# Performance work log

Measured on AMD Instinct MI355X. Metric: run time of the kernel, lower is better.

The kernel has to match this reference:

```python
import jax, jax.numpy as jnp
import numpy as np

L, D, H, DK, S, B = 6, 1024, 16, 64, 512, 8
DFF = 4 * D
NEG = -1.0e9


def layer_norm(x, g, b, eps=1e-5):
    mu = jnp.mean(x, axis=-1, keepdims=True)
    var = jnp.var(x, axis=-1, keepdims=True)
    return (x - mu) * jax.lax.rsqrt(var + eps) * g + b


def setup_inputs() -> dict:
    key = jax.random.key(0)
    ks = jax.random.split(key, 16)
    s = 0.02
    inp = {
        "x": jax.random.normal(ks[0], (B, S, D), jnp.float32),
        "mask": jax.random.bernoulli(ks[1], 0.1, (B, S, S)),
        "relation": jax.random.normal(ks[2], (B, S, S), jnp.float32) * 0.1,
        # per-layer params (stacked over L)
        "Wq": jax.random.normal(ks[3], (L, D, H * DK), jnp.float32) * s,
        "Wk": jax.random.normal(ks[4], (L, D, H * DK), jnp.float32) * s,
        "Wv": jax.random.normal(ks[5], (L, D, H * DK), jnp.float32) * s,
        "Wo": jax.random.normal(ks[6], (L, H * DK, D), jnp.float32) * s,
        "bo": jnp.zeros((L, D), jnp.float32),
        "ln_g": jnp.ones((L, D), jnp.float32),   # EncoderLayer.norm (shared pre-attn / pre-FFN)
        "ln_b": jnp.zeros((L, D), jnp.float32),
        "ln2_g": jnp.ones((L, D), jnp.float32),  # AttSubLayerv2.norm
        "ln2_b": jnp.zeros((L, D), jnp.float32),
        "W1": jax.random.normal(ks[7], (L, D, DFF), jnp.float32) * s,
        "b1": jnp.zeros((L, DFF), jnp.float32),
        "W2": jax.random.normal(ks[8], (L, DFF, D), jnp.float32) * s,
        "b2": jnp.zeros((L, D), jnp.float32),
        "lnf_g": jnp.ones((D,), jnp.float32),    # Encoder.norm
        "lnf_b": jnp.zeros((D,), jnp.float32),
    }
    return inp


def reference(x, mask, relation, Wq, Wk, Wv, Wo, bo, ln_g, ln_b, ln2_g, ln2_b,
              W1, b1, W2, b2, lnf_g, lnf_b):
    # dropout layers run in eval mode (identity)
    scale = 1.0 / jnp.sqrt(jnp.asarray(DK, x.dtype))
    h = x
    attns = []
    for l in range(L):
        q_in = layer_norm(h, ln_g[l], ln_b[l])
        # AttSubLayerv2
        def proj(W):
            return jnp.einsum('bsd,de->bse', q_in, W).reshape(h.shape[0], -1, H, DK).transpose(0, 2, 1, 3)
        Q, K, V = proj(Wq[l]), proj(Wk[l]), proj(Wv[l])  # [B,H,S,DK]
        qk = jnp.einsum('bhqd,bhkd->bhqk', Q, K)
        scores = jnp.einsum('bhqk,bkn->bhqn', qk, relation) * scale
        scores = jnp.where(mask[:, None], NEG, scores)
        p = jax.nn.softmax(scores, axis=-1)  # [B,H,S,S]
        att = jnp.einsum('bhqk,bhkd->bhqd', p, V).transpose(0, 2, 1, 3).reshape(h.shape[0], -1, H * DK)
        att = att @ Wo[l] + bo[l]
        att_out = layer_norm(att + q_in, ln2_g[l], ln2_b[l])
        h = h + att_out
        # FFN (pre-norm with shared EncoderLayer norm)
        f = layer_norm(h, ln_g[l], ln_b[l])
        h = h + (jax.nn.relu(f @ W1[l] + b1[l]) @ W2[l] + b2[l])
        attns.append(p)
    out = layer_norm(h, lnf_g, lnf_b)
    return out, jnp.stack(attns)
```

## Files before the change

### kernel.cpp

```cpp
#include <hip/hip_runtime.h>
#include <hip/hip_bf16.h>
#include <stdint.h>

#define LL 6
#define DD 1024
#define HH 16
#define DKK 64
#define SS 512
#define BB 8
#define DFF_ 4096
#define BS (BB*SS)
#define NEGV -1.0e9f

typedef __attribute__((ext_vector_type(8))) short short8;
typedef __attribute__((ext_vector_type(4))) float f32x4;
typedef __attribute__((ext_vector_type(4))) unsigned short ushort4v;

static __device__ __forceinline__ float bf2f(unsigned short u){
  union { unsigned int i; float f; } v; v.i = ((unsigned int)u)<<16; return v.f;
}
static __device__ __forceinline__ unsigned short f2bf(float f){
  union { float f; unsigned int i; } v; v.f=f;
  unsigned int r = v.i + 0x7fff + ((v.i>>16)&1);
  return (unsigned short)(r>>16);
}

static __device__ __forceinline__ void gload16(const void* g, void* l){
  __builtin_amdgcn_global_load_lds((const __attribute__((address_space(1))) unsigned int*)g,
                                   (__attribute__((address_space(3))) unsigned int*)l, 16, 0, 0);
}

struct TrDesc { const float* in; unsigned short* out; long is1,is2,os1,os2; int ldin,ldout,zd,gx,gy; };
struct TrPack { TrDesc d[7]; int cum[8]; };

__global__ void __launch_bounds__(256) tr_multi_k(TrPack P)
{
  __shared__ float t[32][33];
  int bid=blockIdx.x, di=0;
  #pragma unroll
  for(int k=1;k<7;k++) if(bid>=P.cum[k]) di=k;
  TrDesc dd=P.d[di];
  int local=bid-P.cum[di];
  int bx=local%dd.gx; int rest=local/dd.gx;
  int by=rest%dd.gy; int z=rest/dd.gy;
  int z1=z/dd.zd, z2=z%dd.zd;
  const float* ip=dd.in+z1*dd.is1+z2*dd.is2;
  unsigned short* op=dd.out+z1*dd.os1+z2*dd.os2;
  int r0=by*32, c0=bx*32;
  int tx=threadIdx.x, ty=threadIdx.y;
  #pragma unroll
  for(int i=0;i<4;i++)
    t[ty+i*8][tx] = ip[(long)(r0+ty+i*8)*dd.ldin + c0+tx];
  __syncthreads();
  #pragma unroll
  for(int i=0;i<4;i++)
    op[(long)(c0+ty+i*8)*dd.ldout + r0+tx] = f2bf(t[tx][ty+i*8]);
}

__global__ void __launch_bounds__(256) maskpack_k(const int* __restrict__ mask, unsigned* __restrict__ mb)
{
  int idx = blockIdx.x*256 + threadIdx.x;
  int row = idx>>4, w = idx&15;
  const int* mp = mask + (long)row*SS + w*32;
  unsigned v=0;
  #pragma unroll
  for(int i=0;i<32;i++) v |= (mp[i]!=0) ? (1u<<i) : 0u;
  mb[idx]=v;
}

__global__ void __launch_bounds__(256) ln_k(const float* __restrict__ src,
    const float* __restrict__ gw, const float* __restrict__ bw,
    float* __restrict__ outf, unsigned short* __restrict__ outb,
    const float* __restrict__ resid)
{
  long row=blockIdx.x;
  float4 v=((const float4*)(src+row*DD))[threadIdx.x];
  float s=v.x+v.y+v.z+v.w;
  float s2=v.x*v.x+v.y*v.y+v.z*v.z+v.w*v.w;
  #pragma unroll
  for(int o=32;o;o>>=1){ s+=__shfl_xor(s,o); s2+=__shfl_xor(s2,o); }
  __shared__ float red[8];
  int wid=threadIdx.x>>6, lane=threadIdx.x&63;
  if(lane==0){ red[wid]=s; red[4+wid]=s2; }
  __syncthreads();
  s=red[0]+red[1]+red[2]+red[3];
  s2=red[4]+red[5]+red[6]+red[7];
  float mu=s*(1.f/DD);
  float rstd=rsqrtf(s2*(1.f/DD)-mu*mu+1e-5f);
  int c=threadIdx.x*4;
  float4 g4=*(const float4*)(gw+c), b4=*(const float4*)(bw+c);
  float4 o;
  o.x=(v.x-mu)*rstd*g4.x+b4.x;
  o.y=(v.y-mu)*rstd*g4.y+b4.y;
  o.z=(v.z-mu)*rstd*g4.z+b4.z;
  o.w=(v.w-mu)*rstd*g4.w+b4.w;
  if(resid){
    float4 r4=((const float4*)(resid+row*DD))[threadIdx.x];
    o.x+=r4.x; o.y+=r4.y; o.z+=r4.z; o.w+=r4.w;
  }
  if(outf) ((float4*)(outf+row*DD))[threadIdx.x]=o;
  if(outb){
    uint2 pk;
    pk.x=(unsigned)f2bf(o.x)|((unsigned)f2bf(o.y)<<16);
    pk.y=(unsigned)f2bf(o.z)|((unsigned)f2bf(o.w)<<16);
    ((uint2*)(outb+row*DD))[threadIdx.x]=pk;
  }
}

__global__ void __launch_bounds__(256) ln2_k(const float* __restrict__ src,
    const float* __restrict__ resid,
    const float* __restrict__ g2, const float* __restrict__ b2,
    const float* __restrict__ g1, const float* __restrict__ b1,
    float* __restrict__ outf, unsigned short* __restrict__ outb)
{
  long row=blockIdx.x;
  int wid=threadIdx.x>>6, lane=threadIdx.x&63, c=threadIdx.x*4;
  __shared__ float red[8];
  float4 v=((const float4*)(src+row*DD))[threadIdx.x];
  float s=v.x+v.y+v.z+v.w;
  float s2=v.x*v.x+v.y*v.y+v.z*v.z+v.w*v.w;
  #pragma unroll
  for(int o=32;o;o>>=1){ s+=__shfl_xor(s,o); s2+=__shfl_xor(s2,o); }
  if(lane==0){ red[wid]=s; red[4+wid]=s2; }
  __syncthreads();
  s=red[0]+red[1]+red[2]+red[3];
  s2=red[4]+red[5]+red[6]+red[7];
  float mu=s*(1.f/DD);
  float rstd=rsqrtf(s2*(1.f/DD)-mu*mu+1e-5f);
  float4 g4=*(const float4*)(g2+c), b4=*(const float4*)(b2+c);
  float4 r4=((const float4*)(resid+row*DD))[threadIdx.x];
  float4 o;
  o.x=(v.x-mu)*rstd*g4.x+b4.x+r4.x;
  o.y=(v.y-mu)*rstd*g4.y+b4.y+r4.y;
  o.z=(v.z-mu)*rstd*g4.z+b4.z+r4.z;
  o.w=(v.w-mu)*rstd*g4.w+b4.w+r4.w;
  ((float4*)(outf+row*DD))[threadIdx.x]=o;
  s=o.x+o.y+o.z+o.w;
  s2=o.x*o.x+o.y*o.y+o.z*o.z+o.w*o.w;
  #pragma unroll
  for(int of=32;of;of>>=1){ s+=__shfl_xor(s,of); s2+=__shfl_xor(s2,of); }
  __syncthreads();
  if(lane==0){ red[wid]=s; red[4+wid]=s2; }
  __syncthreads();
  s=red[0]+red[1]+red[2]+red[3];
  s2=red[4]+red[5]+red[6]+red[7];
  mu=s*(1.f/DD);
  rstd=rsqrtf(s2*(1.f/DD)-mu*mu+1e-5f);
  g4=*(const float4*)(g1+c); b4=*(const float4*)(b1+c);
  uint2 pk;
  pk.x=(unsigned)f2bf((o.x-mu)*rstd*g4.x+b4.x)|((unsigned)f2bf((o.y-mu)*rstd*g4.y+b4.y)<<16);
  pk.y=(unsigned)f2bf((o.z-mu)*rstd*g4.z+b4.z)|((unsigned)f2bf((o.w-mu)*rstd*g4.w+b4.w)<<16);
  ((uint2*)(outb+row*DD))[threadIdx.x]=pk;
}

struct GemmP {
  const unsigned short* A; long sA1,sA2; int ldA;
  const unsigned short* B; long sB1,sB2; int ldB;
  float* outF; unsigned short* outB; long sO1,sO2; int ldO;
  const float* bias;
  const float* residF; long sR1,sR2; int ldR;
  const unsigned short* residB;
  unsigned short *kt, *vt;
  int K, ZD, relu, qkv;
};

template<int BM,int BN,int WM,int WN>
__global__ void __launch_bounds__(WM*WN*64) gemm_k(GemmP p)
{
  constexpr int BK=32, NT=WM*WN*64;
  constexpr int FM=BM/WM/16, FN=BN/WN/16;
  __shared__ __align__(16) unsigned short As[BM*BK];
  __shared__ __align__(16) unsigned short Bs[BN*BK];
  int z=blockIdx.z, z1=z/p.ZD, z2=z%p.ZD;
  const unsigned short* Ap = p.A + z1*p.sA1 + z2*p.sA2;
  const unsigned short* Bp = p.B + z1*p.sB1 + z2*p.sB2;
  int m0=blockIdx.y*BM, n0=blockIdx.x*BN;
  int tid=threadIdx.x, lane=tid&63, wid=tid>>6;
  int wr=wid/WN, wc=wid%WN;
  f32x4 acc[FM][FN];
  #pragma unroll
  for(int i=0;i<FM;i++)
    #pragma unroll
    for(int j=0;j<FN;j++) acc[i][j]=(f32x4){0.f,0.f,0.f,0.f};
  const int lr=lane&15, lk=(lane>>4)*8;
  for(int k0=0;k0<p.K;k0+=BK){
    #pragma unroll
    for(int r=0;r<(BM*4)/NT;r++){
      int v=r*NT+wid*64+lane;
      gload16(Ap + (long)(m0+(v>>2))*p.ldA + k0 + (v&3)*8, As + (r*NT+wid*64)*8);
    }
    #pragma unroll
    for(int r=0;r<(BN*4)/NT;r++){
      int v=r*NT+wid*64+lane;
      gload16(Bp + (long)(n0+(v>>2))*p.ldB + k0 + (v&3)*8, Bs + (r*NT+wid*64)*8);
    }
    __syncthreads();
    short8 af[FM], bfr[FN];
    #pragma unroll
    for(int i=0;i<FM;i++) af[i]=*(const short8*)(As + (wr*(BM/WM)+i*16+lr)*BK + lk);
    #pragma unroll
    for(int j=0;j<FN;j++) bfr[j]=*(const short8*)(Bs + (wc*(BN/WN)+j*16+lr)*BK + lk);
    #pragma unroll
    for(int i=0;i<FM;i++)
      #pragma unroll
      for(int j=0;j<FN;j++)
        acc[i][j]=__builtin_amdgcn_mfma_f32_16x16x32_bf16(af[i],bfr[j],acc[i][j],0,0,0);
    __syncthreads();
  }
  int rl=(lane>>4)*4;
  if(p.qkv){
    #pragma unroll
    for(int i=0;i<FM;i++){
      int gr0 = m0 + wr*(BM/WM) + i*16 + rl;
      int b = gr0>>9, s0 = gr0&511;
      #pragma unroll
      for(int j=0;j<FN;j++){
        int gcb = n0 + wc*(BN/WN) + j*16;
        int gc = gcb + lr;
        if(gcb < 1024){
          #pragma unroll
          for(int r=0;r<4;r++)
            p.outB[(long)(gr0+r)*1024 + gc] = f2bf(acc[i][j][r]);
        } else {
          unsigned short* dst = gcb<2048 ? p.kt : p.vt;
          int hh=(gc>>6)&15, d=gc&63;
          ushort4v pk;
          pk.x=f2bf(acc[i][j][0]); pk.y=f2bf(acc[i][j][1]);
          pk.z=f2bf(acc[i][j][2]); pk.w=f2bf(acc[i][j][3]);
          *(ushort4v*)(dst + (((long)b*HH+hh)*DKK+d)*SS + s0) = pk;
        }
      }
    }
    return;
  }
  #pragma unroll
  for(int i=0;i<FM;i++){
    int gr0 = m0 + wr*(BM/WM) + i*16 + rl;
    #pragma unroll
    for(int j=0;j<FN;j++){
      int gc = n0 + wc*(BN/WN) + j*16 + lr;
      float bv = p.bias ? p.bias[gc] : 0.f;
      #pragma unroll
      for(int r=0;r<4;r++){
        long ro=(long)(gr0+r);
        float val=acc[i][j][r]+bv;
        if(p.relu) val=fmaxf(val,0.f);
        if(p.residF) val += p.residF[z1*p.sR1+z2*p.sR2+ro*(long)p.ldR+gc];
        if(p.residB) val += bf2f(p.residB[ro*(long)p.ldR+gc]);
        long oo = z1*p.sO1+z2*p.sO2+ro*(long)p.ldO+gc;
        if(p.outF) p.outF[oo]=val;
        if(p.outB) p.outB[oo]=f2bf(val);
      }
    }
  }
}

template<int BM,int BN,int WM,int WN>
static inline void launch_gemm(const GemmP& p,int M,int N,int Z,hipStream_t s){
  gemm_k<BM,BN,WM,WN><<<dim3(N/BN,M/BM,Z),dim3(WM*WN*64),0,s>>>(p);
}

__global__ void __launch_bounds__(512) att_k(const unsigned short* __restrict__ Qb,
    const unsigned short* __restrict__ KRT, float* __restrict__ pout,
    const unsigned* __restrict__ maskb, const unsigned short* __restrict__ Vt,
    unsigned short* __restrict__ attb)
{
  constexpr int BM=128, BK=32, NT=512;
  constexpr int FM=4, FN=8;
  __shared__ __align__(16) char smem[49152];
  unsigned short* As = (unsigned short*)smem;
  unsigned short* Bs = (unsigned short*)(smem+8192);
  unsigned short* Ps = (unsigned short*)smem;
  unsigned short* Vs = (unsigned short*)(smem+32768);
  __shared__ float redmx[BM][4];
  __shared__ float redsm[BM][4];
  int bh = blockIdx.y; int b = bh>>4, h = bh&15;
  const unsigned short* Ap = Qb + (long)b*SS*1024 + h*64;
  const unsigned short* Bp = KRT + (long)bh*SS*DKK;
  int m0 = blockIdx.x*BM;
  int tid=threadIdx.x, lane=tid&63, wid=tid>>6;
  int wr=wid>>2, wc=wid&3;
  f32x4 acc[FM][FN];
  #pragma unroll
  for(int i=0;i<FM;i++)
    #pragma unroll
    for(int j=0;j<FN;j++) acc[i][j]=(f32x4){0.f,0.f,0.f,0.f};
  const int lr=lane&15, lk=(lane>>4)*8;
  for(int k0=0;k0<DKK;k0+=BK){
    { int v=tid;
      gload16(Ap + (long)(m0+(v>>2))*1024 + k0 + (v&3)*8, As + (wid*64)*8); }
    #pragma unroll
    for(int r=0;r<4;r++){
      int v=r*NT+tid;
      gload16(Bp + (long)(v>>2)*DKK + k0 + (v&3)*8, Bs + (r*NT+wid*64)*8);
    }
    __syncthreads();
    short8 af[FM], bfr[FN];
    #pragma unroll
    for(int i=0;i<FM;i++) af[i]=*(const short8*)(As + (wr*64+i*16+lr)*BK + lk);
    #pragma unroll
    for(int j=0;j<FN;j++) bfr[j]=*(const short8*)(Bs + (wc*128+j*16+lr)*BK + lk);
    #pragma unroll
    for(int i=0;i<FM;i++)
      #pragma unroll
      for(int j=0;j<FN;j++)
        acc[i][j]=__builtin_amdgcn_mfma_f32_16x16x32_bf16(af[i],bfr[j],acc[i][j],0,0,0);
    __syncthreads();
  }
  const int rl=(lane>>4)*4;
  #pragma unroll
  for(int i=0;i<FM;i++){
    #pragma unroll
    for(int r=0;r<4;r++){
      int row=wr*64+i*16+rl+r;
      uint4 mw = *((const uint4*)(maskb + ((long)(b*SS+m0+row))*16 + wc*4));
      float m_=-3.4e38f;
      #pragma unroll
      for(int j=0;j<FN;j++){
        unsigned word = (j>>1)==0? mw.x : (j>>1)==1? mw.y : (j>>1)==2? mw.z : mw.w;
        float v = ((word>>(((j&1)<<4)+lr))&1) ? NEGV : acc[i][j][r]*0.125f;
        acc[i][j][r]=v; m_=fmaxf(m_,v);
      }
      #pragma unroll
      for(int o=1;o<16;o<<=1) m_=fmaxf(m_,__shfl_xor(m_,o));
      if(lr==0) redmx[row][wc]=m_;
    }
  }
  __syncthreads();
  #pragma unroll
  for(int i=0;i<FM;i++){
    #pragma unroll
    for(int r=0;r<4;r++){
      int row=wr*64+i*16+rl+r;
      float m_=fmaxf(fmaxf(redmx[row][0],redmx[row][1]),fmaxf(redmx[row][2],redmx[row][3]));
      float s_=0.f;
      #pragma unroll
      for(int j=0;j<FN;j++){
        float e=__expf(acc[i][j][r]-m_);
        acc[i][j][r]=e; s_+=e;
      }
      #pragma unroll
      for(int o=1;o<16;o<<=1) s_+=__shfl_xor(s_,o);
      if(lr==0) redsm[row][wc]=s_;
    }
  }
  __syncthreads();
  #pragma unroll
  for(int i=0;i<FM;i++){
    #pragma unroll
    for(int r=0;r<4;r++){
      int row=wr*64+i*16+rl+r;
      float inv=1.f/(redsm[row][0]+redsm[row][1]+redsm[row][2]+redsm[row][3]);
      long obase=((long)bh*SS + m0+row)*(long)SS;
      #pragma unroll
      for(int j=0;j<FN;j++){
        int col=wc*128+j*16+lr;
        float pv=acc[i][j][r]*inv;
        acc[i][j][r]=pv;
        pout[obase+col]=pv;
      }
    }
  }
  __syncthreads();
  f32x4 attacc[4];
  #pragma unroll
  for(int j=0;j<4;j++) attacc[j]=(f32x4){0.f,0.f,0.f,0.f};
  for(int kc=0;kc<4;kc++){
    #pragma unroll
    for(int r2=0;r2<2;r2++){
      int v=r2*512+tid;
      int d=v>>4, m=v&15;
      int u=m^(d&7);
      gload16(Vt + ((long)bh*64 + d)*512 + kc*128 + u*8, Vs + (r2*512 + wid*64)*8);
    }
    if(wc==kc){
      #pragma unroll
      for(int i=0;i<FM;i++){
        #pragma unroll
        for(int r=0;r<4;r++){
          int row=wr*64+i*16+rl+r;
          #pragma unroll
          for(int j=0;j<FN;j++){
            int col=j*16+lr;
            Ps[row*128 + (col ^ ((row&7)<<3))] = f2bf(acc[i][j][r]);
          }
        }
      }
    }
    __syncthreads();
    #pragma unroll
    for(int kk=0;kk<4;kk++){
      int arow=wid*16+lr;
      short8 paf=*(const short8*)(Ps + arow*128 + ((kk*32+lk) ^ ((arow&7)<<3)));
      #pragma unroll
      for(int j=0;j<4;j++){
        int d=j*16+lr;
        short8 vbf=*(const short8*)(Vs + d*128 + ((kk*32+lk) ^ ((d&7)<<3)));
        attacc[j]=__builtin_amdgcn_mfma_f32_16x16x32_bf16(paf,vbf,attacc[j],0,0,0);
      }
    }
    __syncthreads();
  }
  #pragma unroll
  for(int j=0;j<4;j++){
    #pragma unroll
    for(int r=0;r<4;r++){
      int row = m0 + wid*16 + rl + r;
      attb[((long)b*SS + row)*DD + h*64 + j*16 + lr] = f2bf(attacc[j][r]);
    }
  }
}

extern "C" void kernel_launch(void* const* d_in, const int* in_sizes, int n_in,
                              void* d_out, int out_size, void* d_ws, size_t ws_size,
                              hipStream_t stream)
{
  const float* x    =(const float*)d_in[0];
  const int*   mask =(const int*)d_in[1];
  const float* rel  =(const float*)d_in[2];
  const float* Wq   =(const float*)d_in[3];
  const float* Wk   =(const float*)d_in[4];
  const float* Wv   =(const float*)d_in[5];
  const float* Wo   =(const float*)d_in[6];
  const float* bo   =(const float*)d_in[7];
  const float* ln_g =(const float*)d_in[8];
  const float* ln_b =(const float*)d_in[9];
  const float* ln2_g=(const float*)d_in[10];
  const float* ln2_b=(const float*)d_in[11];
  const float* W1   =(const float*)d_in[12];
  const float* b1   =(const float*)d_in[13];
  const float* W2   =(const float*)d_in[14];
  const float* b2   =(const float*)d_in[15];
  const float* lnf_g=(const float*)d_in[16];
  const float* lnf_b=(const float*)d_in[17];
  float* out=(float*)d_out;

  char* w=(char*)d_ws;
  auto alloc=[&](long bytes)->void*{ void* p=(void*)w; w += (bytes+255)&~255L; return p; };
  unsigned short* WTqkv=(unsigned short*)alloc((long)LL*3072*1024*2);
  unsigned short* WoT  =(unsigned short*)alloc((long)LL*1024*1024*2);
  unsigned short* W1T  =(unsigned short*)alloc((long)LL*DFF_*DD*2);
  unsigned short* W2T  =(unsigned short*)alloc((long)LL*DD*DFF_*2);
  unsigned short* relT =(unsigned short*)alloc((long)BB*SS*SS*2);
  unsigned short* qin_b=(unsigned short*)alloc((long)BS*DD*2);
  unsigned short* Qb   =(unsigned short*)alloc((long)BS*1024*2);
  unsigned short* Vt   =(unsigned short*)alloc((long)BB*HH*DKK*SS*2);
  unsigned short* Kt   =(unsigned short*)alloc((long)BB*HH*DKK*SS*2);
  unsigned short* KRT  =(unsigned short*)alloc((long)BB*HH*SS*DKK*2);
  unsigned short* attb =(unsigned short*)alloc((long)BS*DD*2);
  float*          attres=(float*)alloc((long)BS*DD*4);
  unsigned short* gbuf =(unsigned short*)alloc((long)BS*DFF_*2);
  float*          hbuf =(float*)alloc((long)BS*DD*4);
  unsigned*       maskb=(unsigned*)alloc((long)BS*16*4);
  (void)ws_size; (void)in_sizes; (void)n_in; (void)out_size;

  TrPack tp;
  auto set=[&](int i, const float* in, unsigned short* o, int ldin, int ldout,
               long is1, long os1, int zd, long is2, long os2, int gx, int gy){
    tp.d[i]={in,o,is1,is2,os1,os2,ldin,ldout,zd,gx,gy};
  };
  set(0, Wq, WTqkv,           1024,1024,(long)1024*1024,(long)3072*1024,1,0,0, 32,32);
  set(1, Wk, WTqkv+1024*1024, 1024,1024,(long)1024*1024,(long)3072*1024,1,0,0, 32,32);
  set(2, Wv, WTqkv+2048*1024, 1024,1024,(long)1024*1024,(long)3072*1024,1,0,0, 32,32);
  set(3, Wo, WoT,             1024,1024,(long)1024*1024,(long)1024*1024,1,0,0, 32,32);
  set(4, W1, W1T, 4096,1024,(long)1024*4096,(long)1024*4096,1,0,0, 128,32);
  set(5, W2, W2T, 1024,4096,(long)4096*1024,(long)4096*1024,1,0,0, 32,128);
  set(6, rel, relT, 512,512,(long)512*512,(long)512*512,1,0,0, 16,16);
  int nb[7]={32*32*LL,32*32*LL,32*32*LL,32*32*LL,128*32*LL,32*128*LL,16*16*BB};
  tp.cum[0]=0;
  for(int i=0;i<7;i++) tp.cum[i+1]=tp.cum[i]+nb[i];
  tr_multi_k<<<dim3(tp.cum[7]),dim3(32,8),0,stream>>>(tp);
  maskpack_k<<<dim3(BS*16/256),dim3(256),0,stream>>>(mask, maskb);

  const float* hin = x;
  for(int l=0;l<LL;l++){
    ln_k<<<dim3(BS),dim3(256),0,stream>>>(hin, ln_g+l*DD, ln_b+l*DD, (float*)nullptr, qin_b, (const float*)nullptr);
    { GemmP p{}; p.A=qin_b; p.ldA=DD; p.B=WTqkv+(long)l*3072*1024; p.ldB=DD;
      p.outB=Qb; p.kt=Kt; p.vt=Vt; p.qkv=1; p.K=DD; p.ZD=1;
      launch_gemm<128,128,2,2>(p, BS, 3072, 1, stream); }
    { GemmP p{}; p.A=relT; p.sA1=(long)SS*SS; p.sA2=0; p.ldA=SS;
      p.B=Kt; p.sB1=(long)HH*DKK*SS; p.sB2=(long)DKK*SS; p.ldB=SS;
      p.outB=KRT; p.sO1=(long)HH*SS*DKK; p.sO2=(long)SS*DKK; p.ldO=DKK;
      p.K=SS; p.ZD=HH;
      launch_gemm<128,64,2,2>(p, SS, DKK, BB*HH, stream); }
    float* attn_l = out + (long)BS*DD + (long)l*BB*HH*SS*SS;
    att_k<<<dim3(SS/128, BB*HH),dim3(512),0,stream>>>(Qb, KRT, attn_l, maskb, Vt, attb);
    { GemmP p{}; p.A=attb; p.ldA=DD; p.B=WoT+(long)l*1024*1024; p.ldB=DD;
      p.outF=attres; p.ldO=DD; p.bias=bo+l*DD;
      p.residB=qin_b; p.ldR=DD; p.K=DD; p.ZD=1;
      launch_gemm<64,128,2,2>(p, BS, DD, 1, stream); }
    ln2_k<<<dim3(BS),dim3(256),0,stream>>>(attres, hin, ln2_g+l*DD, ln2_b+l*DD,
        ln_g+l*DD, ln_b+l*DD, hbuf, qin_b);
    { GemmP p{}; p.A=qin_b; p.ldA=DD; p.B=W1T+(long)l*DFF_*DD; p.ldB=DD;
      p.outB=gbuf; p.ldO=DFF_; p.bias=b1+l*DFF_; p.relu=1; p.K=DD; p.ZD=1;
      launch_gemm<128,128,2,2>(p, BS, DFF_, 1, stream); }
    { GemmP p{}; p.A=gbuf; p.ldA=DFF_; p.B=W2T+(long)l*DD*DFF_; p.ldB=DFF_;
      p.outF=hbuf; p.ldO=DD; p.bias=b2+l*DD;
      p.residF=hbuf; p.ldR=DD; p.K=DFF_; p.ZD=1;
      launch_gemm<64,128,2,2>(p, BS, DD, 1, stream); }
    hin=hbuf;
  }
  ln_k<<<dim3(BS),dim3(256),0,stream>>>(hbuf, lnf_g, lnf_b, out, (unsigned short*)nullptr, (const float*)nullptr);
}
```

Measured before the change: 2.390 ms.

## Add triple-buffered 128x256 GEMM with swizzled LDS for dense projections

Adds a new bf16 MFMA GEMM kernel that uses 128x256 tiles with BK=64 and 8 waves. It keeps three LDS stages in flight with manual vmcnt waits and raw barriers, and XOR-swizzles the LDS columns to avoid bank conflicts. The QKV, Wo, W1 and W2 projections are routed to this kernel, and the QKV scatter epilogue moves out of the generic GEMM into it. Deeper prefetch and larger tiles are meant to hide global-load latency and raise MFMA utilisation, at the cost of more LDS per block and fewer blocks for the N=1024 GEMMs (4x32 grid).

```diff
diff --git a/kernel.cpp b/kernel.cpp
--- a/kernel.cpp
+++ b/kernel.cpp
@@ -208,31 +208,6 @@
     __syncthreads();
   }
   int rl=(lane>>4)*4;
-  if(p.qkv){
-    #pragma unroll
-    for(int i=0;i<FM;i++){
-      int gr0 = m0 + wr*(BM/WM) + i*16 + rl;
-      int b = gr0>>9, s0 = gr0&511;
-      #pragma unroll
-      for(int j=0;j<FN;j++){
-        int gcb = n0 + wc*(BN/WN) + j*16;
-        int gc = gcb + lr;
-        if(gcb < 1024){
-          #pragma unroll
-          for(int r=0;r<4;r++)
-            p.outB[(long)(gr0+r)*1024 + gc] = f2bf(acc[i][j][r]);
-        } else {
-          unsigned short* dst = gcb<2048 ? p.kt : p.vt;
-          int hh=(gc>>6)&15, d=gc&63;
-          ushort4v pk;
-          pk.x=f2bf(acc[i][j][0]); pk.y=f2bf(acc[i][j][1]);
-          pk.z=f2bf(acc[i][j][2]); pk.w=f2bf(acc[i][j][3]);
-          *(ushort4v*)(dst + (((long)b*HH+hh)*DKK+d)*SS + s0) = pk;
-        }
-      }
-    }
-    return;
-  }
   #pragma unroll
   for(int i=0;i<FM;i++){
     int gr0 = m0 + wr*(BM/WM) + i*16 + rl;
@@ -258,6 +233,141 @@
 template<int BM,int BN,int WM,int WN>
 static inline void launch_gemm(const GemmP& p,int M,int N,int Z,hipStream_t s){
   gemm_k<BM,BN,WM,WN><<<dim3(N/BN,M/BM,Z),dim3(WM*WN*64),0,s>>>(p);
+}
+
+template<int MODE>
+__global__ void __launch_bounds__(512,2) gemm8_k(GemmP p)
+{
+  constexpr int BM=128, BN=256, BK=64;
+  constexpr int BUFE=(BM+BN)*BK;
+  __shared__ __align__(16) unsigned short smem[3*BUFE];
+  const int tid=threadIdx.x, lane=tid&63, wid=tid>>6;
+  const int wr=wid>>2, wc=wid&3;
+  const int lr=lane&15, lk=(lane>>4)*8;
+  const int m0=blockIdx.y*BM, n0=blockIdx.x*BN;
+  const int NT=p.K/BK;
+  const unsigned short* Ap=p.A;
+  const unsigned short* Bp=p.B;
+
+  const int sr8 = lane>>3;
+  const int scol = ((lane&7)*8) ^ ((sr8&4)?16:0);
+
+  #define STAGE8(T,BI) { \
+    const long kb_=(long)(T)*BK; \
+    unsigned short* As_=smem+(BI)*BUFE; \
+    unsigned short* Bs_=As_+BM*BK; \
+    _Pragma("unroll") \
+    for(int L=0;L<2;L++){ \
+      int r_=L*64+wid*8+sr8; \
+      gload16(Ap+(long)(m0+r_)*p.ldA+kb_+scol, As_+L*4096+wid*512); \
+    } \
+    _Pragma("unroll") \
+    for(int L=0;L<4;L++){ \
+      int r_=L*64+wid*8+sr8; \
+      gload16(Bp+(long)(n0+r_)*p.ldB+kb_+scol, Bs_+L*4096+wid*512); \
+    } }
+
+  f32x4 acc[4][4];
+  #pragma unroll
+  for(int m=0;m<4;m++)
+    #pragma unroll
+    for(int n=0;n<4;n++) acc[m][n]=(f32x4){0.f,0.f,0.f,0.f};
+
+  STAGE8(0,0);
+  STAGE8(1,1);
+  asm volatile("s_waitcnt vmcnt(6)" ::: "memory");
+  __builtin_amdgcn_sched_barrier(0);
+  __builtin_amdgcn_s_barrier();
+  __builtin_amdgcn_sched_barrier(0);
+
+  const int xr = (lr&4)?16:0;
+  for(int t=0;t<NT;t++){
+    if(t+2<NT) STAGE8(t+2,(t+2)%3);
+    const unsigned short* As=smem+(t%3)*BUFE;
+    const unsigned short* Bs=As+BM*BK;
+    short8 a[4][2], b[4][2];
+    #pragma unroll
+    for(int m=0;m<4;m++){
+      int r=wr*64+m*16+lr;
+      #pragma unroll
+      for(int kk=0;kk<2;kk++)
+        a[m][kk]=*(const short8*)(As + r*BK + ((kk*32+lk)^xr));
+    }
+    #pragma unroll
+    for(int n=0;n<4;n++){
+      int c=wc*64+n*16+lr;
+      #pragma unroll
+      for(int kk=0;kk<2;kk++)
+        b[n][kk]=*(const short8*)(Bs + c*BK + ((kk*32+lk)^xr));
+    }
+    __builtin_amdgcn_s_setprio(1);
+    #pragma unroll
+    for(int kk=0;kk<2;kk++)
+      #pragma unroll
+      for(int m=0;m<4;m++)
+        #pragma unroll
+        for(int n=0;n<4;n++)
+          acc[m][n]=__builtin_amdgcn_mfma_f32_16x16x32_bf16(a[m][kk],b[n][kk],acc[m][n],0,0,0);
+    __builtin_amdgcn_s_setprio(0);
+    if(t+2<NT) asm volatile("s_waitcnt vmcnt(6)" ::: "memory");
+    else       asm volatile("s_waitcnt vmcnt(0)" ::: "memory");
+    __builtin_amdgcn_sched_barrier(0);
+    __builtin_amdgcn_s_barrier();
+    __builtin_amdgcn_sched_barrier(0);
+  }
+  #undef STAGE8
+
+  const int rl=(lane>>4)*4;
+  if(MODE==1){
+    int sec = n0>>10;
+    #pragma unroll
+    for(int m=0;m<4;m++){
+      int gr0 = m0 + wr*64 + m*16 + rl;
+      int b = gr0>>9, s0 = gr0&511;
+      #pragma unroll
+      for(int n=0;n<4;n++){
+        int gc = n0 + wc*64 + n*16 + lr;
+        if(sec==0){
+          #pragma unroll
+          for(int r=0;r<4;r++)
+            p.outB[(long)(gr0+r)*1024 + gc] = f2bf(acc[m][n][r]);
+        } else {
+          unsigned short* dst = sec==1 ? p.kt : p.vt;
+          int hh=(gc>>6)&15, d=gc&63;
+          ushort4v pk;
+          pk.x=f2bf(acc[m][n][0]); pk.y=f2bf(acc[m][n][1]);
+          pk.z=f2bf(acc[m][n][2]); pk.w=f2bf(acc[m][n][3]);
+          *(ushort4v*)(dst + (((long)b*HH+hh)*DKK+d)*SS + s0) = pk;
+        }
+      }
+    }
+  } else {
+    #pragma unroll
+    for(int m=0;m<4;m++){
+      int gr0 = m0 + wr*64 + m*16 + rl;
+      #pragma unroll
+      for(int n=0;n<4;n++){
+        int gc = n0 + wc*64 + n*16 + lr;
+        float bv = p.bias ? p.bias[gc] : 0.f;
+        #pragma unroll
+        for(int r=0;r<4;r++){
+          long ro=(long)(gr0+r);
+          float val=acc[m][n][r]+bv;
+          if(p.relu) val=fmaxf(val,0.f);
+          if(p.residF) val += p.residF[ro*(long)p.ldR+gc];
+          if(p.residB) val += bf2f(p.residB[ro*(long)p.ldR+gc]);
+          long oo = ro*(long)p.ldO+gc;
+          if(p.outF) p.outF[oo]=val;
+          if(p.outB) p.outB[oo]=f2bf(val);
+        }
+      }
+    }
+  }
+}
+
+template<int MODE>
+static inline void launch_gemm8(const GemmP& p,int M,int N,hipStream_t s){
+  gemm8_k<MODE><<<dim3(N/256,M/128),dim3(512),0,s>>>(p);
 }
 
 __global__ void __launch_bounds__(512) att_k(const unsigned short* __restrict__ Qb,
@@ -476,8 +586,8 @@
   for(int l=0;l<LL;l++){
     ln_k<<<dim3(BS),dim3(256),0,stream>>>(hin, ln_g+l*DD, ln_b+l*DD, (float*)nullptr, qin_b, (const float*)nullptr);
     { GemmP p{}; p.A=qin_b; p.ldA=DD; p.B=WTqkv+(long)l*3072*1024; p.ldB=DD;
-      p.outB=Qb; p.kt=Kt; p.vt=Vt; p.qkv=1; p.K=DD; p.ZD=1;
-      launch_gemm<128,128,2,2>(p, BS, 3072, 1, stream); }
+      p.outB=Qb; p.kt=Kt; p.vt=Vt; p.K=DD;
+      launch_gemm8<1>(p, BS, 3072, stream); }
     { GemmP p{}; p.A=relT; p.sA1=(long)SS*SS; p.sA2=0; p.ldA=SS;
       p.B=Kt; p.sB1=(long)HH*DKK*SS; p.sB2=(long)DKK*SS; p.ldB=SS;
       p.outB=KRT; p.sO1=(long)HH*SS*DKK; p.sO2=(long)SS*DKK; p.ldO=DKK;
@@ -487,17 +597,17 @@
     att_k<<<dim3(SS/128, BB*HH),dim3(512),0,stream>>>(Qb, KRT, attn_l, maskb, Vt, attb);
     { GemmP p{}; p.A=attb; p.ldA=DD; p.B=WoT+(long)l*1024*1024; p.ldB=DD;
       p.outF=attres; p.ldO=DD; p.bias=bo+l*DD;
-      p.residB=qin_b; p.ldR=DD; p.K=DD; p.ZD=1;
-      launch_gemm<64,128,2,2>(p, BS, DD, 1, stream); }
+      p.residB=qin_b; p.ldR=DD; p.K=DD;
+      launch_gemm8<0>(p, BS, DD, stream); }
     ln2_k<<<dim3(BS),dim3(256),0,stream>>>(attres, hin, ln2_g+l*DD, ln2_b+l*DD,
         ln_g+l*DD, ln_b+l*DD, hbuf, qin_b);
     { GemmP p{}; p.A=qin_b; p.ldA=DD; p.B=W1T+(long)l*DFF_*DD; p.ldB=DD;
-      p.outB=gbuf; p.ldO=DFF_; p.bias=b1+l*DFF_; p.relu=1; p.K=DD; p.ZD=1;
-      launch_gemm<128,128,2,2>(p, BS, DFF_, 1, stream); }
+      p.outB=gbuf; p.ldO=DFF_; p.bias=b1+l*DFF_; p.relu=1; p.K=DD;
+      launch_gemm8<0>(p, BS, DFF_, stream); }
     { GemmP p{}; p.A=gbuf; p.ldA=DFF_; p.B=W2T+(long)l*DD*DFF_; p.ldB=DFF_;
       p.outF=hbuf; p.ldO=DD; p.bias=b2+l*DD;
-      p.residF=hbuf; p.ldR=DD; p.K=DFF_; p.ZD=1;
-      launch_gemm<64,128,2,2>(p, BS, DD, 1, stream); }
+      p.residF=hbuf; p.ldR=DD; p.K=DFF_;
+      launch_gemm8<0>(p, BS, DD, stream); }
     hin=hbuf;
   }
   ln_k<<<dim3(BS),dim3(256),0,stream>>>(hbuf, lnf_g, lnf_b, out, (unsigned short*)nullptr, (const float*)nullptr);
```

Result: faster. 2.236 ms (-6.4%).

## Rewrite GEMM with double-buffered LDS, XOR swizzle, larger tiles, grouped block order

Applied to the files above, without the earlier changes.

Replaces the single-buffered BK=32 GEMM with a double-buffered BK=64 kernel. The next K tile is prefetched while MFMAs run on the current one, LDS is XOR-swizzled to avoid bank conflicts, and a remapped 1D grid groups blocks for better L2 reuse. Larger 256x256 tiles with 8 waves are used for the QKV and FFN1 GEMMs. The relation x K GEMM is batched per batch across all heads, writing KRT in a [B,S,1024] layout that att_k now reads with stride 1024. This adds more LDS per block and more register pressure from the larger tiles, which may limit occupancy.

```diff
diff --git a/kernel.cpp b/kernel.cpp
--- a/kernel.cpp
+++ b/kernel.cpp
@@ -154,110 +154,143 @@
 }
 
 struct GemmP {
-  const unsigned short* A; long sA1,sA2; int ldA;
-  const unsigned short* B; long sB1,sB2; int ldB;
-  float* outF; unsigned short* outB; long sO1,sO2; int ldO;
+  const unsigned short* A; long sA1; int ldA;
+  const unsigned short* B; long sB1; int ldB;
+  float* outF; unsigned short* outB; long sO1; int ldO;
   const float* bias;
-  const float* residF; long sR1,sR2; int ldR;
+  const float* residF; int ldR;
   const unsigned short* residB;
   unsigned short *kt, *vt;
-  int K, ZD, relu, qkv;
+  int K, relu, mb;
 };
 
-template<int BM,int BN,int WM,int WN>
-__global__ void __launch_bounds__(WM*WN*64) gemm_k(GemmP p)
-{
-  constexpr int BK=32, NT=WM*WN*64;
-  constexpr int FM=BM/WM/16, FN=BN/WN/16;
-  __shared__ __align__(16) unsigned short As[BM*BK];
-  __shared__ __align__(16) unsigned short Bs[BN*BK];
-  int z=blockIdx.z, z1=z/p.ZD, z2=z%p.ZD;
-  const unsigned short* Ap = p.A + z1*p.sA1 + z2*p.sA2;
-  const unsigned short* Bp = p.B + z1*p.sB1 + z2*p.sB2;
-  int m0=blockIdx.y*BM, n0=blockIdx.x*BN;
-  int tid=threadIdx.x, lane=tid&63, wid=tid>>6;
-  int wr=wid/WN, wc=wid%WN;
+template<int MODE,int BM,int BN,int WM,int WN>
+__global__ void __launch_bounds__(WM*WN*64,2) gemm2p_k(GemmP p)
+{
+  constexpr int NW=WM*WN, BK=64;
+  constexpr int WRT=BM/WM, WCT=BN/WN;
+  constexpr int FM=WRT/16, FN=WCT/16;
+  constexpr int RG=NW*8;
+  constexpr int BUFE=(BM+BN)*BK;
+  __shared__ __align__(16) unsigned short smem[2*BUFE];
+  const int tid=threadIdx.x, lane=tid&63, wid=tid>>6;
+  const int wr=wid/WN, wc=wid%WN;
+  const int lr=lane&15, lk=(lane>>4)*8;
+  const int nwg=gridDim.x, bid=blockIdx.x;
+  const int nb=(bid&7)*(nwg>>3)+(bid>>3);
+  const int m0=(nb%p.mb)*BM, n0=(nb/p.mb)*BN;
+  const int z=blockIdx.y;
+  const unsigned short* Ap=p.A+(long)z*p.sA1;
+  const unsigned short* Bp=p.B+(long)z*p.sB1;
+  const int NT=p.K/BK;
+
+  const int sr8=lane>>3;
+  const int scol=((lane&7)^sr8)<<3;
+
+  #define STG(T,BI) { \
+    const long kb_=(long)(T)*BK; \
+    unsigned short* As_=smem+(BI)*BUFE; \
+    unsigned short* Bs_=As_+BM*BK; \
+    _Pragma("unroll") \
+    for(int L=0;L<BM/RG;L++){ int r_=L*RG+wid*8+sr8; \
+      gload16(Ap+(long)(m0+r_)*p.ldA+kb_+scol, As_+(L*RG+wid*8)*BK); } \
+    _Pragma("unroll") \
+    for(int L=0;L<BN/RG;L++){ int r_=L*RG+wid*8+sr8; \
+      gload16(Bp+(long)(n0+r_)*p.ldB+kb_+scol, Bs_+(L*RG+wid*8)*BK); } }
+
   f32x4 acc[FM][FN];
   #pragma unroll
-  for(int i=0;i<FM;i++)
-    #pragma unroll
-    for(int j=0;j<FN;j++) acc[i][j]=(f32x4){0.f,0.f,0.f,0.f};
-  const int lr=lane&15, lk=(lane>>4)*8;
-  for(int k0=0;k0<p.K;k0+=BK){
-    #pragma unroll
-    for(int r=0;r<(BM*4)/NT;r++){
-      int v=r*NT+wid*64+lane;
-      gload16(Ap + (long)(m0+(v>>2))*p.ldA + k0 + (v&3)*8, As + (r*NT+wid*64)*8);
-    }
-    #pragma unroll
-    for(int r=0;r<(BN*4)/NT;r++){
-      int v=r*NT+wid*64+lane;
-      gload16(Bp + (long)(n0+(v>>2))*p.ldB + k0 + (v&3)*8, Bs + (r*NT+wid*64)*8);
-    }
-    __syncthreads();
-    short8 af[FM], bfr[FN];
-    #pragma unroll
-    for(int i=0;i<FM;i++) af[i]=*(const short8*)(As + (wr*(BM/WM)+i*16+lr)*BK + lk);
-    #pragma unroll
-    for(int j=0;j<FN;j++) bfr[j]=*(const short8*)(Bs + (wc*(BN/WN)+j*16+lr)*BK + lk);
-    #pragma unroll
-    for(int i=0;i<FM;i++)
-      #pragma unroll
-      for(int j=0;j<FN;j++)
-        acc[i][j]=__builtin_amdgcn_mfma_f32_16x16x32_bf16(af[i],bfr[j],acc[i][j],0,0,0);
-    __syncthreads();
-  }
-  int rl=(lane>>4)*4;
-  if(p.qkv){
-    #pragma unroll
-    for(int i=0;i<FM;i++){
-      int gr0 = m0 + wr*(BM/WM) + i*16 + rl;
+  for(int m=0;m<FM;m++)
+    #pragma unroll
+    for(int n=0;n<FN;n++) acc[m][n]=(f32x4){0.f,0.f,0.f,0.f};
+
+  STG(0,0);
+  asm volatile("s_waitcnt vmcnt(0)" ::: "memory");
+  __builtin_amdgcn_sched_barrier(0);
+  __builtin_amdgcn_s_barrier();
+  __builtin_amdgcn_sched_barrier(0);
+
+  const int xr=(lr&7)<<3;
+  int cur=0;
+  for(int t=0;t<NT;t++){
+    if(t+1<NT) STG(t+1,cur^1);
+    const unsigned short* As=smem+cur*BUFE;
+    const unsigned short* Bs=As+BM*BK;
+    #pragma unroll
+    for(int kk=0;kk<2;kk++){
+      short8 a[FM], b[FN];
+      #pragma unroll
+      for(int m=0;m<FM;m++) a[m]=*(const short8*)(As+(wr*WRT+m*16+lr)*BK+((kk*32+lk)^xr));
+      #pragma unroll
+      for(int n=0;n<FN;n++) b[n]=*(const short8*)(Bs+(wc*WCT+n*16+lr)*BK+((kk*32+lk)^xr));
+      __builtin_amdgcn_s_setprio(1);
+      #pragma unroll
+      for(int m=0;m<FM;m++)
+        #pragma unroll
+        for(int n=0;n<FN;n++)
+          acc[m][n]=__builtin_amdgcn_mfma_f32_16x16x32_bf16(a[m],b[n],acc[m][n],0,0,0);
+      __builtin_amdgcn_s_setprio(0);
+    }
+    asm volatile("s_waitcnt vmcnt(0)" ::: "memory");
+    __builtin_amdgcn_sched_barrier(0);
+    __builtin_amdgcn_s_barrier();
+    __builtin_amdgcn_sched_barrier(0);
+    cur^=1;
+  }
+  #undef STG
+
+  const int rl=(lane>>4)*4;
+  if(MODE==1){
+    int sec = n0>>10;
+    #pragma unroll
+    for(int m=0;m<FM;m++){
+      int gr0 = m0 + wr*WRT + m*16 + rl;
       int b = gr0>>9, s0 = gr0&511;
       #pragma unroll
-      for(int j=0;j<FN;j++){
-        int gcb = n0 + wc*(BN/WN) + j*16;
-        int gc = gcb + lr;
-        if(gcb < 1024){
+      for(int n=0;n<FN;n++){
+        int gc = n0 + wc*WCT + n*16 + lr;
+        if(sec==0){
           #pragma unroll
           for(int r=0;r<4;r++)
-            p.outB[(long)(gr0+r)*1024 + gc] = f2bf(acc[i][j][r]);
+            p.outB[(long)(gr0+r)*1024 + gc] = f2bf(acc[m][n][r]);
         } else {
-          unsigned short* dst = gcb<2048 ? p.kt : p.vt;
+          unsigned short* dst = sec==1 ? p.kt : p.vt;
           int hh=(gc>>6)&15, d=gc&63;
           ushort4v pk;
-          pk.x=f2bf(acc[i][j][0]); pk.y=f2bf(acc[i][j][1]);
-          pk.z=f2bf(acc[i][j][2]); pk.w=f2bf(acc[i][j][3]);
+          pk.x=f2bf(acc[m][n][0]); pk.y=f2bf(acc[m][n][1]);
+          pk.z=f2bf(acc[m][n][2]); pk.w=f2bf(acc[m][n][3]);
           *(ushort4v*)(dst + (((long)b*HH+hh)*DKK+d)*SS + s0) = pk;
         }
       }
     }
-    return;
-  }
-  #pragma unroll
-  for(int i=0;i<FM;i++){
-    int gr0 = m0 + wr*(BM/WM) + i*16 + rl;
-    #pragma unroll
-    for(int j=0;j<FN;j++){
-      int gc = n0 + wc*(BN/WN) + j*16 + lr;
-      float bv = p.bias ? p.bias[gc] : 0.f;
-      #pragma unroll
-      for(int r=0;r<4;r++){
-        long ro=(long)(gr0+r);
-        float val=acc[i][j][r]+bv;
-        if(p.relu) val=fmaxf(val,0.f);
-        if(p.residF) val += p.residF[z1*p.sR1+z2*p.sR2+ro*(long)p.ldR+gc];
-        if(p.residB) val += bf2f(p.residB[ro*(long)p.ldR+gc]);
-        long oo = z1*p.sO1+z2*p.sO2+ro*(long)p.ldO+gc;
-        if(p.outF) p.outF[oo]=val;
-        if(p.outB) p.outB[oo]=f2bf(val);
-      }
-    }
-  }
-}
-
-template<int BM,int BN,int WM,int WN>
-static inline void launch_gemm(const GemmP& p,int M,int N,int Z,hipStream_t s){
-  gemm_k<BM,BN,WM,WN><<<dim3(N/BN,M/BM,Z),dim3(WM*WN*64),0,s>>>(p);
+  } else {
+    #pragma unroll
+    for(int m=0;m<FM;m++){
+      int gr0 = m0 + wr*WRT + m*16 + rl;
+      #pragma unroll
+      for(int n=0;n<FN;n++){
+        int gc = n0 + wc*WCT + n*16 + lr;
+        float bv = p.bias ? p.bias[gc] : 0.f;
+        #pragma unroll
+        for(int r=0;r<4;r++){
+          long ro=(long)(gr0+r);
+          float val=acc[m][n][r]+bv;
+          if(p.relu) val=fmaxf(val,0.f);
+          if(p.residF) val += p.residF[ro*(long)p.ldR+gc];
+          if(p.residB) val += bf2f(p.residB[ro*(long)p.ldR+gc]);
+          long oo = (long)z*p.sO1 + ro*(long)p.ldO+gc;
+          if(p.outF) p.outF[oo]=val;
+          if(p.outB) p.outB[oo]=f2bf(val);
+        }
+      }
+    }
+  }
+}
+
+template<int MODE,int BM,int BN,int WM,int WN>
+static inline void launch_gemm2p(GemmP& p,int M,int N,int Z,hipStream_t s){
+  p.mb=M/BM;
+  gemm2p_k<MODE,BM,BN,WM,WN><<<dim3((M/BM)*(N/BN),Z),dim3(WM*WN*64),0,s>>>(p);
 }
 
 __global__ void __launch_bounds__(512) att_k(const unsigned short* __restrict__ Qb,
@@ -276,7 +309,7 @@
   __shared__ float redsm[BM][4];
   int bh = blockIdx.y; int b = bh>>4, h = bh&15;
   const unsigned short* Ap = Qb + (long)b*SS*1024 + h*64;
-  const unsigned short* Bp = KRT + (long)bh*SS*DKK;
+  const unsigned short* Bp = KRT + (long)b*SS*1024 + h*64;
   int m0 = blockIdx.x*BM;
   int tid=threadIdx.x, lane=tid&63, wid=tid>>6;
   int wr=wid>>2, wc=wid&3;
@@ -292,7 +325,7 @@
     #pragma unroll
     for(int r=0;r<4;r++){
       int v=r*NT+tid;
-      gload16(Bp + (long)(v>>2)*DKK + k0 + (v&3)*8, Bs + (r*NT+wid*64)*8);
+      gload16(Bp + (long)(v>>2)*1024 + k0 + (v&3)*8, Bs + (r*NT+wid*64)*8);
     }
     __syncthreads();
     short8 af[FM], bfr[FN];
@@ -446,7 +479,7 @@
   unsigned short* Qb   =(unsigned short*)alloc((long)BS*1024*2);
   unsigned short* Vt   =(unsigned short*)alloc((long)BB*HH*DKK*SS*2);
   unsigned short* Kt   =(unsigned short*)alloc((long)BB*HH*DKK*SS*2);
-  unsigned short* KRT  =(unsigned short*)alloc((long)BB*HH*SS*DKK*2);
+  unsigned short* KRT  =(unsigned short*)alloc((long)BB*SS*1024*2);
   unsigned short* attb =(unsigned short*)alloc((long)BS*DD*2);
   float*          attres=(float*)alloc((long)BS*DD*4);
   unsigned short* gbuf =(unsigned short*)alloc((long)BS*DFF_*2);
@@ -476,28 +509,27 @@
   for(int l=0;l<LL;l++){
     ln_k<<<dim3(BS),dim3(256),0,stream>>>(hin, ln_g+l*DD, ln_b+l*DD, (float*)nullptr, qin_b, (const float*)nullptr);
     { GemmP p{}; p.A=qin_b; p.ldA=DD; p.B=WTqkv+(long)l*3072*1024; p.ldB=DD;
-      p.outB=Qb; p.kt=Kt; p.vt=Vt; p.qkv=1; p.K=DD; p.ZD=1;
-      launch_gemm<128,128,2,2>(p, BS, 3072, 1, stream); }
-    { GemmP p{}; p.A=relT; p.sA1=(long)SS*SS; p.sA2=0; p.ldA=SS;
-      p.B=Kt; p.sB1=(long)HH*DKK*SS; p.sB2=(long)DKK*SS; p.ldB=SS;
-      p.outB=KRT; p.sO1=(long)HH*SS*DKK; p.sO2=(long)SS*DKK; p.ldO=DKK;
-      p.K=SS; p.ZD=HH;
-      launch_gemm<128,64,2,2>(p, SS, DKK, BB*HH, stream); }
+      p.outB=Qb; p.kt=Kt; p.vt=Vt; p.K=DD;
+      launch_gemm2p<1,256,256,2,4>(p, BS, 3072, 1, stream); }
+    { GemmP p{}; p.A=relT; p.sA1=(long)SS*SS; p.ldA=SS;
+      p.B=Kt; p.sB1=(long)HH*DKK*SS; p.ldB=SS;
+      p.outB=KRT; p.sO1=(long)SS*1024; p.ldO=1024; p.K=SS;
+      launch_gemm2p<0,128,128,2,2>(p, SS, 1024, BB, stream); }
     float* attn_l = out + (long)BS*DD + (long)l*BB*HH*SS*SS;
     att_k<<<dim3(SS/128, BB*HH),dim3(512),0,stream>>>(Qb, KRT, attn_l, maskb, Vt, attb);
     { GemmP p{}; p.A=attb; p.ldA=DD; p.B=WoT+(long)l*1024*1024; p.ldB=DD;
       p.outF=attres; p.ldO=DD; p.bias=bo+l*DD;
-      p.residB=qin_b; p.ldR=DD; p.K=DD; p.ZD=1;
-      launch_gemm<64,128,2,2>(p, BS, DD, 1, stream); }
+      p.residB=qin_b; p.ldR=DD; p.K=DD;
+      launch_gemm2p<0,128,128,2,2>(p, BS, DD, 1, stream); }
     ln2_k<<<dim3(BS),dim3(256),0,stream>>>(attres, hin, ln2_g+l*DD, ln2_b+l*DD,
         ln_g+l*DD, ln_b+l*DD, hbuf, qin_b);
     { GemmP p{}; p.A=qin_b; p.ldA=DD; p.B=W1T+(long)l*DFF_*DD; p.ldB=DD;
-      p.outB=gbuf; p.ldO=DFF_; p.bias=b1+l*DFF_; p.relu=1; p.K=DD; p.ZD=1;
-      launch_gemm<128,128,2,2>(p, BS, DFF_, 1, stream); }
+      p.outB=gbuf; p.ldO=DFF_; p.bias=b1+l*DFF_; p.relu=1; p.K=DD;
+      launch_gemm2p<0,256,256,2,4>(p, BS, DFF_, 1, stream); }
     { GemmP p{}; p.A=gbuf; p.ldA=DFF_; p.B=W2T+(long)l*DD*DFF_; p.ldB=DFF_;
       p.outF=hbuf; p.ldO=DD; p.bias=b2+l*DD;
-      p.residF=hbuf; p.ldR=DD; p.K=DFF_; p.ZD=1;
-      launch_gemm<64,128,2,2>(p, BS, DD, 1, stream); }
+      p.residF=hbuf; p.ldR=DD; p.K=DFF_;
+      launch_gemm2p<0,128,128,2,2>(p, BS, DD, 1, stream); }
     hin=hbuf;
   }
   ln_k<<<dim3(BS),dim3(256),0,stream>>>(hbuf, lnf_g, lnf_b, out, (unsigned short*)nullptr, (const float*)nullptr);
```

Result: faster. 2.205 ms (-7.8%).
